# Kernel optimization log

Hardware: AMD Instinct MI355X
Metric: run time of the kernel (lower is better)

## Reference

```python
import jax, jax.numpy as jnp
import numpy as np

V, H, B, T = 128, 1024, 64, 256


def setup_inputs() -> dict:
    key = jax.random.key(0)
    ks = jax.random.split(key, 16)
    s = 0.02
    rn = lambda k, shp: (jax.random.normal(k, shp, jnp.float32) * s)
    return {
        "x": jax.random.normal(ks[0], (1, T, B, V), jnp.float32),
        "hA": jax.random.normal(ks[1], (B, H), jnp.float32),
        "cA": jax.random.normal(ks[2], (B, H), jnp.float32),
        "hB": jax.random.normal(ks[3], (B, H), jnp.float32),
        "cB": jax.random.normal(ks[4], (B, H), jnp.float32),
        "WA1": rn(ks[5], (4 * H, V)), "bA1": rn(ks[6], (4 * H,)),
        "WA2": rn(ks[7], (4 * H, H)), "bA2": rn(ks[8], (4 * H,)),
        "WB1": rn(ks[9], (4 * H, H)), "bB1": rn(ks[10], (4 * H,)),
        "WB2": rn(ks[11], (4 * H, H)), "bB2": rn(ks[12], (4 * H,)),
        "Wfc": jax.random.uniform(ks[13], (V, H), jnp.float32, -1.0, 1.0),
        "bfc": jnp.zeros((V,), jnp.float32),
    }


def _lstm_cell(x, h, c, W1, b1, W2, b2):
    # gates = Linear1(x) + Linear2(h); chunk order: in, forget, cell, out
    g = x @ W1.T + b1 + h @ W2.T + b2  # [B, 4H]
    i, f, cc, o = jnp.split(g, 4, axis=1)
    c_new = jax.nn.sigmoid(f) * c + jax.nn.sigmoid(i) * jnp.tanh(cc)
    h_new = jax.nn.sigmoid(o) * jnp.tanh(c_new)
    return h_new, c_new


def reference(x, hA, cA, hB, cB, WA1, bA1, WA2, bA2, WB1, bB1, WB2, bB2, Wfc, bfc):
    seq = x[0]  # [T, B, V], matches x.unbind(0)[0]

    def step(carry, xt):
        hA, cA, hB, cB = carry
        hA, cA = _lstm_cell(xt, hA, cA, WA1, bA1, WA2, bA2)
        hB, cB = _lstm_cell(hA, hB, cB, WB1, bB1, WB2, bB2)
        return (hA, cA, hB, cB), hB

    (hA, cA, hB, cB), outs = jax.lax.scan(step, (hA, cA, hB, cB), seq)
    # dropout is identity at inference (eval mode)
    out = outs.reshape(T * B, H) @ Wfc.T + bfc  # [T*B, V]
    return (out, hA, cA, hB, cB)
```

## Files before the change

kernel.cpp:

```cpp
#include <hip/hip_runtime.h>

#define VD 128
#define HD 1024
#define BD 64
#define TD 256
#define NB 256

typedef __bf16 bf16;
typedef __bf16 bf16x8 __attribute__((ext_vector_type(8)));
typedef __bf16 bf16x4 __attribute__((ext_vector_type(4)));
typedef float f32x4 __attribute__((ext_vector_type(4)));

#define OFF_OUTS 0ull
#define OFF_XW   33554432ull
#define OFF_WA1  (OFF_XW  + 4194304ull)
#define OFF_WA2  (OFF_WA1 + 1048576ull)
#define OFF_WB1  (OFF_WA2 + 8388608ull)
#define OFF_WB2  (OFF_WB1 + 8388608ull)
#define OFF_WFC  (OFF_WB2 + 8388608ull)
#define OFF_BUFA (OFF_WFC + 262144ull)
#define OFF_BUFB (OFF_BUFA + 262144ull)
#define OFF_CAF  (OFF_BUFB + 262144ull)
#define OFF_CBF  (OFF_CAF + 262144ull)
#define OFF_HAST (OFF_CBF + 262144ull)
#define HAST_BYTES (257ull * BD * HD * 2ull)


#define SMEM_BYTES 87040

#define BAR_WORDS 8192
#define SPIN_CAP (1 << 16)

struct Params {
  const bf16 *x, *WA1, *WA2, *WB1, *WB2;
  const float *bA1, *bA2, *bB1, *bB2;
  bf16 *bufA, *bufB, *outs;
  float *cA, *cB;
};

struct PParams {
  const bf16 *x, *WA1, *WA2, *WB1, *WB2;
  const float *bA1, *bA2, *bB1, *bB2;
  const bf16 *hBinit;
  bf16 *hAst, *outs;
  float *cA, *cB;
};

__device__ __forceinline__ bf16x8 ld8(const bf16* p) {
  return *reinterpret_cast<const bf16x8*>(p);
}
__device__ __forceinline__ float sigf(float x) { return 1.f / (1.f + __expf(-x)); }

__device__ __forceinline__ void st_dev_bf16(bf16* p, float f) {
  unsigned v = (unsigned)__builtin_bit_cast(unsigned short, (bf16)f);
  asm volatile("global_store_short %0, %1, off sc0 sc1" :: "v"(p), "v"(v) : "memory");
}

__global__ void conv_k(const float* x, const float* WA1, const float* WA2,
                       const float* WB1, const float* WB2, const float* Wfc,
                       char* ws, int sm) {
  const size_t g4 = (size_t)blockIdx.x * 256 + threadIdx.x;
  size_t i = g4 * 4;
  if (i < 2097152ull) {
    float4 v = *reinterpret_cast<const float4*>(x + i);
    bf16x4 o = { (bf16)v.x, (bf16)v.y, (bf16)v.z, (bf16)v.w };
    bf16* dst = (bf16*)(ws + OFF_XW);
    if (sm) {
      size_t t = i >> 13, r = i & 8191, b = r >> 7, vv = r & 127;
      *reinterpret_cast<bf16x4*>(dst + t * 8192 + ((vv >> 5) << 11) + (b << 5) + (vv & 31)) = o;
    } else {
      *reinterpret_cast<bf16x4*>(dst + i) = o;
    }
    return;
  }
  const float* src;
  bf16* dst;
  size_t off;
  if (i < 2621440ull)        { src = WA1; dst = (bf16*)(ws + OFF_WA1); off = i - 2097152ull; }
  else if (i < 6815744ull)   { src = WA2; dst = (bf16*)(ws + OFF_WA2); off = i - 2621440ull; }
  else if (i < 11010048ull)  { src = WB1; dst = (bf16*)(ws + OFF_WB1); off = i - 6815744ull; }
  else if (i < 15204352ull)  { src = WB2; dst = (bf16*)(ws + OFF_WB2); off = i - 11010048ull; }
  else if (i < 15335424ull)  { src = Wfc; dst = (bf16*)(ws + OFF_WFC); off = i - 15204352ull; }
  else return;
  float4 v = *reinterpret_cast<const float4*>(src + off);
  bf16x4 o = { (bf16)v.x, (bf16)v.y, (bf16)v.z, (bf16)v.w };
  *reinterpret_cast<bf16x4*>(dst + off) = o;
}

__global__ void init_k(const float* hA, const float* cA, const float* hB, const float* cB,
                       char* ws, unsigned* bar, int sm) {
  int i = blockIdx.x * 256 + threadIdx.x;
  if (i < BAR_WORDS) bar[i] = 0u;
  ((float*)(ws + OFF_CAF))[i] = cA[i];
  ((float*)(ws + OFF_CBF))[i] = cB[i];
  ((bf16*)(ws + OFF_BUFB))[i] = (bf16)hB[i];
  if (sm) {
    int b = i >> 10, j = i & 1023;
    int tix = ((j >> 5) << 11) + (b << 5) + (j & 31);
    ((bf16*)(ws + OFF_HAST))[tix] = (bf16)hA[i];
    ((bf16*)(ws + OFF_BUFA))[tix] = (bf16)hB[i];
  } else {
    ((bf16*)(ws + OFF_BUFA))[i] = (bf16)hA[i];
  }
}

__global__ void __launch_bounds__(512, 2) persist_k(PParams p, unsigned* bar) {
  extern __shared__ char smem[];
  float (*part)[8][16][65] = (float (*)[8][16][65])smem;

  const int tid = threadIdx.x;
  const int wv = tid >> 6, lane = tid & 63;
  const int lrow = lane & 15, q = lane >> 4;
  const int j0 = blockIdx.x * 4;
  const int grow = (lrow >> 2) * HD + j0 + (lrow & 3);
  const int mrow = lrow << 5;
  const int kbase = wv * 128;

  bf16x8 wa2[4], wb1[4], wb2[4], wa1 = {};
#pragma unroll
  for (int g = 0; g < 4; g++) {
    const size_t ko = (size_t)grow * HD + kbase + g * 32 + q * 8;
    wa2[g] = ld8(p.WA2 + ko);
    wb1[g] = ld8(p.WB1 + ko);
    wb2[g] = ld8(p.WB2 + ko);
  }
  if (wv < 4) wa1 = ld8(p.WA1 + (size_t)grow * VD + wv * 32 + q * 8);

  const int ejj = tid & 3;
  const int eb = (tid >> 2) & 63;
  const int ecs = tid >> 8;
  const int ej = j0 + ejj;
  const int eidx = eb * HD + ej;
  const int etix = ((ej >> 5) << 11) + (eb << 5) + (ej & 31);
  const float* b1 = ecs ? p.bB1 : p.bA1;
  const float* b2 = ecs ? p.bB2 : p.bA2;
  float* ec = ecs ? p.cB : p.cA;
  float bsum[4];
#pragma unroll
  for (int g = 0; g < 4; g++) bsum[g] = b1[g * HD + ej] + b2[g * HD + ej];
  float creg = ec[eidx];

  __syncthreads();

  for (int t = 0; t <= TD; t++) {
    const bool doA = (t < TD), doB = (t >= 1);
    const bf16* hA = p.hAst + (size_t)t * 65536;
    const bf16* hAg = hA + wv * 8192 + q * 8;
    f32x4 accA[4] = {};
    f32x4 accB[4] = {};
    bf16x8 af[4];
#pragma unroll
    for (int g = 0; g < 4; g++) {
#pragma unroll
      for (int m = 0; m < 4; m++)
        af[m] = ld8(hAg + g * 2048 + m * 512 + mrow);
      if (doA)
#pragma unroll
        for (int m = 0; m < 4; m++)
          accA[m] = __builtin_amdgcn_mfma_f32_16x16x32_bf16(af[m], wa2[g], accA[m], 0, 0, 0);
      if (doB)
#pragma unroll
        for (int m = 0; m < 4; m++)
          accB[m] = __builtin_amdgcn_mfma_f32_16x16x32_bf16(af[m], wb1[g], accB[m], 0, 0, 0);
    }
    if (doA && wv < 4) {
      const bf16* xb = p.x + (size_t)t * 8192 + wv * 2048 + q * 8;
#pragma unroll
      for (int m = 0; m < 4; m++) {
        bf16x8 xf = ld8(xb + m * 512 + mrow);
        accA[m] = __builtin_amdgcn_mfma_f32_16x16x32_bf16(xf, wa1, accA[m], 0, 0, 0);
      }
    }
    if (doB) {
      const bf16* hBb = (t == 1) ? p.hBinit : p.outs + (size_t)(t - 2) * 65536;
      const bf16* hBg = hBb + wv * 8192 + q * 8;
#pragma unroll
      for (int g = 0; g < 4; g++) {
#pragma unroll
        for (int m = 0; m < 4; m++) {
          bf16x8 bf_ = ld8(hBg + g * 2048 + m * 512 + mrow);
          accB[m] = __builtin_amdgcn_mfma_f32_16x16x32_bf16(bf_, wb2[g], accB[m], 0, 0, 0);
        }
      }
    }
    if (doA)
#pragma unroll
      for (int m = 0; m < 4; m++)
#pragma unroll
        for (int r = 0; r < 4; r++)
          part[0][wv][lrow][m * 16 + q * 4 + r] = accA[m][r];
    if (doB)
#pragma unroll
      for (int m = 0; m < 4; m++)
#pragma unroll
        for (int r = 0; r < 4; r++)
          part[1][wv][lrow][m * 16 + q * 4 + r] = accB[m][r];
    __syncthreads();

    const bool ew = (ecs == 0) ? doA : doB;
    if (ew) {
      float g4[4];
#pragma unroll
      for (int g = 0; g < 4; g++) {
        int n = g * 4 + ejj;
        float s = 0.f;
#pragma unroll
        for (int w = 0; w < 8; w++) s += part[ecs][w][n][eb];
        g4[g] = bsum[g] + s;
      }
      float cn = sigf(g4[1]) * creg + sigf(g4[0]) * tanhf(g4[2]);
      float hn = sigf(g4[3]) * tanhf(cn);
      creg = cn;
      if (ecs == 0) {
        st_dev_bf16(p.hAst + (size_t)(t + 1) * 65536 + etix, hn);
      } else {
        st_dev_bf16(p.outs + (size_t)(t - 1) * 65536 + etix, hn);
      }
    }

    if (t < TD) {
      asm volatile("s_waitcnt vmcnt(0)" ::: "memory");
      __syncthreads();
      const unsigned tgt = (unsigned)(t + 1);
      if (blockIdx.x == 0 && wv == 0) {
        if (lane == 0)
          __hip_atomic_store(&bar[1024], tgt, __ATOMIC_RELAXED, __HIP_MEMORY_SCOPE_AGENT);
        int sp = 0;
        for (;;) {
          unsigned a0 = __hip_atomic_load(&bar[1024 + (lane * 4 + 0) * 16], __ATOMIC_RELAXED, __HIP_MEMORY_SCOPE_AGENT);
          unsigned a1 = __hip_atomic_load(&bar[1024 + (lane * 4 + 1) * 16], __ATOMIC_RELAXED, __HIP_MEMORY_SCOPE_AGENT);
          unsigned a2 = __hip_atomic_load(&bar[1024 + (lane * 4 + 2) * 16], __ATOMIC_RELAXED, __HIP_MEMORY_SCOPE_AGENT);
          unsigned a3 = __hip_atomic_load(&bar[1024 + (lane * 4 + 3) * 16], __ATOMIC_RELAXED, __HIP_MEMORY_SCOPE_AGENT);
          if (__all(a0 >= tgt && a1 >= tgt && a2 >= tgt && a3 >= tgt)) break;
          __builtin_amdgcn_s_sleep(2);
          if (++sp > SPIN_CAP) break;
        }
        __hip_atomic_store(&bar[lane * 16], tgt, __ATOMIC_RELAXED, __HIP_MEMORY_SCOPE_AGENT);
      } else if (tid == 0) {
        __hip_atomic_store(&bar[1024 + blockIdx.x * 16], tgt, __ATOMIC_RELAXED, __HIP_MEMORY_SCOPE_AGENT);
        int sp = 0;
        while (__hip_atomic_load(&bar[(blockIdx.x & 63) * 16], __ATOMIC_RELAXED, __HIP_MEMORY_SCOPE_AGENT) < tgt) {
          __builtin_amdgcn_s_sleep(2);
          if (++sp > SPIN_CAP) break;
        }
      }
      __syncthreads();
    }
  }
  ec[eidx] = creg;
}

__global__ void __launch_bounds__(512) phase_k(Params p, int t) {
  __shared__ float part[8][16][65];
  const int tid = threadIdx.x;
  const int wv = tid >> 6, lane = tid & 63;
  const int lrow = lane & 15, q = lane >> 4;
  const int j0 = blockIdx.x * 4;
  const int cs = wv >> 2, kq = wv & 3;
  const int gate = lrow >> 2, jj = lrow & 3;
  const int grow = gate * HD + j0 + jj;

  const bf16 *w1, *w2;
  if (cs == 0) { w1 = p.WA1 + grow * VD + q * 8; w2 = p.WA2 + (size_t)grow * HD + q * 8; }
  else         { w1 = p.WB1 + (size_t)grow * HD + q * 8; w2 = p.WB2 + (size_t)grow * HD + q * 8; }

  const bool active = (cs == 0) ? (t < TD) : (t >= 1);
  const bf16* hA = p.bufA + ((t & 1) ? (size_t)BD * HD : 0);
  if (active) {
    f32x4 acc[4] = {};
    if (cs == 0) {
      if (kq == 0) {
        const bf16* xb = p.x + (size_t)t * BD * VD + q * 8;
#pragma unroll
        for (int s = 0; s < 4; s++) {
          bf16x8 bfv = ld8(w1 + s * 32);
          const bf16* ap = xb + s * 32;
#pragma unroll
          for (int m = 0; m < 4; m++) {
            bf16x8 afv = ld8(ap + (m * 16 + lrow) * VD);
            acc[m] = __builtin_amdgcn_mfma_f32_16x16x32_bf16(afv, bfv, acc[m], 0, 0, 0);
          }
        }
      }
      const int hk0 = (kq == 0) ? 0 : kq * 288 - 128;
      const int nh = (kq == 0) ? 5 : 9;
#pragma unroll 3
      for (int s = 0; s < nh; s++) {
        int hk = hk0 + s * 32;
        bf16x8 bfv = ld8(w2 + hk);
        const bf16* ap = hA + hk + q * 8;
#pragma unroll
        for (int m = 0; m < 4; m++) {
          bf16x8 afv = ld8(ap + (size_t)(m * 16 + lrow) * HD);
          acc[m] = __builtin_amdgcn_mfma_f32_16x16x32_bf16(afv, bfv, acc[m], 0, 0, 0);
        }
      }
    } else {
      const bf16* hB = p.bufB + (((t - 1) & 1) ? (size_t)BD * HD : 0);
      const bf16* hp = (kq < 2) ? hA : hB;
      const bf16* wp = (kq < 2) ? w1 : w2;
      const int k0 = (kq & 1) * 512;
#pragma unroll 4
      for (int s = 0; s < 16; s++) {
        int hk = k0 + s * 32;
        bf16x8 bfv = ld8(wp + hk);
        const bf16* ap = hp + hk + q * 8;
#pragma unroll
        for (int m = 0; m < 4; m++) {
          bf16x8 afv = ld8(ap + (size_t)(m * 16 + lrow) * HD);
          acc[m] = __builtin_amdgcn_mfma_f32_16x16x32_bf16(afv, bfv, acc[m], 0, 0, 0);
        }
      }
    }
#pragma unroll
    for (int m = 0; m < 4; m++)
#pragma unroll
      for (int r = 0; r < 4; r++)
        part[wv][lrow][m * 16 + q * 4 + r] = acc[m][r];
  }
  __syncthreads();

  const int eb = tid & 63;
  const int ejj = (tid >> 6) & 3;
  const int ecs = tid >> 8;
  const int ej = j0 + ejj;
  const int eidx = eb * HD + ej;
  const bool ew = (ecs == 0) ? (t < TD) : (t >= 1);
  if (ew) {
    const float* b1 = ecs ? p.bB1 : p.bA1;
    const float* b2 = ecs ? p.bB2 : p.bA2;
    float* ec = ecs ? p.cB : p.cA;
    const int wb = ecs * 4;
    float g4[4];
#pragma unroll
    for (int g = 0; g < 4; g++) {
      int n = g * 4 + ejj;
      g4[g] = b1[g * HD + ej] + b2[g * HD + ej] + part[wb + 0][n][eb] +
              part[wb + 1][n][eb] + part[wb + 2][n][eb] + part[wb + 3][n][eb];
    }
    float cold = ec[eidx];
    float cn = sigf(g4[1]) * cold + sigf(g4[0]) * tanhf(g4[2]);
    float hn = sigf(g4[3]) * tanhf(cn);
    ec[eidx] = cn;
    if (ecs == 0) {
      p.bufA[(((t + 1) & 1) ? (size_t)BD * HD : 0) + eidx] = (bf16)hn;
    } else {
      p.bufB[((t & 1) ? (size_t)BD * HD : 0) + eidx] = (bf16)hn;
      p.outs[((size_t)(t - 1) * BD + eb) * HD + ej] = (bf16)hn;
    }
  }
}

__global__ void fc_k(const bf16* outs, const bf16* Wfc, const float* bfc, float* out,
                     int sm) {
  const int tid = threadIdx.x;
  const int wv = tid >> 6, lane = tid & 63;
  const int lrow = lane & 15, q = lane >> 4;
  const int row0 = blockIdx.x * 64 + wv * 16;
  const bf16* arow;
  int astride;
  if (sm) {
    const int bb = wv * 16 + lrow;
    arow = outs + (size_t)blockIdx.x * 65536 + (bb << 5) + q * 8;
    astride = 2048;
  } else {
    arow = outs + (size_t)(row0 + lrow) * HD + q * 8;
    astride = 32;
  }
  const bf16* wrow[8];
#pragma unroll
  for (int ct = 0; ct < 8; ct++) wrow[ct] = Wfc + (size_t)(ct * 16 + lrow) * HD + q * 8;
  f32x4 acc[8] = {};
#pragma unroll 2
  for (int s = 0; s < 32; s++) {
    bf16x8 afv = ld8(arow + (size_t)s * astride);
#pragma unroll
    for (int ct = 0; ct < 8; ct++) {
      bf16x8 bfv = ld8(wrow[ct] + s * 32);
      acc[ct] = __builtin_amdgcn_mfma_f32_16x16x32_bf16(afv, bfv, acc[ct], 0, 0, 0);
    }
  }
#pragma unroll
  for (int ct = 0; ct < 8; ct++) {
    float bv = bfc[ct * 16 + lrow];
#pragma unroll
    for (int r = 0; r < 4; r++)
      out[(size_t)(row0 + q * 4 + r) * VD + ct * 16 + lrow] = acc[ct][r] + bv;
  }
}

__global__ void tail_k(const char* ws, float* out, int sm) {
  int i = blockIdx.x * 256 + threadIdx.x;
  float* o = out + (size_t)TD * BD * VD;
  float hAv, hBv;
  if (sm) {
    int b = i >> 10, j = i & 1023;
    int tix = ((j >> 5) << 11) + (b << 5) + (j & 31);
    hAv = (float)(((const bf16*)(ws + OFF_HAST))[(size_t)TD * 65536 + tix]);
    hBv = (float)(((const bf16*)(ws + OFF_OUTS))[(size_t)(TD - 1) * 65536 + tix]);
  } else {
    hAv = (float)((const bf16*)(ws + OFF_BUFA))[i];
    hBv = (float)((const bf16*)(ws + OFF_BUFB))[i];
  }
  o[i]             = hAv;
  o[65536 + i]     = ((const float*)(ws + OFF_CAF))[i];
  o[2 * 65536 + i] = hBv;
  o[3 * 65536 + i] = ((const float*)(ws + OFF_CBF))[i];
}

extern "C" void kernel_launch(void* const* d_in, const int* in_sizes, int n_in,
                              void* d_out, int out_size, void* d_ws, size_t ws_size,
                              hipStream_t stream) {
  const float* x   = (const float*)d_in[0];
  const float* hA  = (const float*)d_in[1];
  const float* cA  = (const float*)d_in[2];
  const float* hB  = (const float*)d_in[3];
  const float* cB  = (const float*)d_in[4];
  const float* WA1 = (const float*)d_in[5];
  const float* bA1 = (const float*)d_in[6];
  const float* WA2 = (const float*)d_in[7];
  const float* bA2 = (const float*)d_in[8];
  const float* WB1 = (const float*)d_in[9];
  const float* bB1 = (const float*)d_in[10];
  const float* WB2 = (const float*)d_in[11];
  const float* bB2 = (const float*)d_in[12];
  const float* Wfc = (const float*)d_in[13];
  const float* bfc = (const float*)d_in[14];

  char* ws = (char*)d_ws;
  unsigned* bar = (unsigned*)d_out;

  const int sm = (ws_size >= OFF_HAST + HAST_BYTES) ? 1 : 0;

  static bool attr_done = false;
  if (!attr_done) {
    hipFuncSetAttribute((const void*)persist_k,
                        hipFuncAttributeMaxDynamicSharedMemorySize, SMEM_BYTES);
    attr_done = true;
  }

  conv_k<<<(15335424 / 4 + 255) / 256, 256, 0, stream>>>(x, WA1, WA2, WB1, WB2, Wfc, ws, sm);
  init_k<<<256, 256, 0, stream>>>(hA, cA, hB, cB, ws, bar, sm);

  bool used_stream = false;
  if (sm) {
    PParams pp{(const bf16*)(ws + OFF_XW), (const bf16*)(ws + OFF_WA1),
               (const bf16*)(ws + OFF_WA2), (const bf16*)(ws + OFF_WB1),
               (const bf16*)(ws + OFF_WB2),
               bA1, bA2, bB1, bB2,
               (const bf16*)(ws + OFF_BUFA),
               (bf16*)(ws + OFF_HAST), (bf16*)(ws + OFF_OUTS),
               (float*)(ws + OFF_CAF), (float*)(ws + OFF_CBF)};
    persist_k<<<NB, 512, SMEM_BYTES, stream>>>(pp, bar);
    used_stream = (hipGetLastError() == hipSuccess);
  }
  if (!used_stream) {
    Params p{(const bf16*)(ws + OFF_XW), (const bf16*)(ws + OFF_WA1),
             (const bf16*)(ws + OFF_WA2), (const bf16*)(ws + OFF_WB1),
             (const bf16*)(ws + OFF_WB2),
             bA1, bA2, bB1, bB2,
             (bf16*)(ws + OFF_BUFA), (bf16*)(ws + OFF_BUFB), (bf16*)(ws + OFF_OUTS),
             (float*)(ws + OFF_CAF), (float*)(ws + OFF_CBF)};
    for (int t = 0; t <= TD; t++) {
      phase_k<<<NB, 512, 0, stream>>>(p, t);
    }
  }

  fc_k<<<256, 256, 0, stream>>>((const bf16*)(ws + OFF_OUTS), (const bf16*)(ws + OFF_WFC),
                                bfc, (float*)d_out, used_stream ? 1 : 0);
  tail_k<<<256, 256, 0, stream>>>(ws, (float*)d_out, used_stream ? 1 : 0);
}
```

Measured before the change: 2.123 ms.

## Halve persistent LSTM grid by giving each block eight hidden units

```diff
diff --git a/kernel.cpp b/kernel.cpp
--- a/kernel.cpp
+++ b/kernel.cpp
@@ -5,6 +5,7 @@
 #define BD 64
 #define TD 256
 #define NB 256
+#define NBP 128
 
 typedef __bf16 bf16;
 typedef __bf16 bf16x8 __attribute__((ext_vector_type(8)));
@@ -26,7 +27,7 @@
 #define HAST_BYTES (257ull * BD * HD * 2ull)
 
 
-#define SMEM_BYTES 87040
+#define SMEM_BYTES 134144
 
 #define BAR_WORDS 8192
 #define SPIN_CAP (1 << 16)
@@ -106,39 +107,56 @@
 
 __global__ void __launch_bounds__(512, 2) persist_k(PParams p, unsigned* bar) {
   extern __shared__ char smem[];
-  float (*part)[8][16][65] = (float (*)[8][16][65])smem;
+  float (*part)[8][16][131] = (float (*)[8][16][131])smem;
 
   const int tid = threadIdx.x;
   const int wv = tid >> 6, lane = tid & 63;
   const int lrow = lane & 15, q = lane >> 4;
-  const int j0 = blockIdx.x * 4;
-  const int grow = (lrow >> 2) * HD + j0 + (lrow & 3);
+  const int j0 = blockIdx.x * 8;
   const int mrow = lrow << 5;
   const int kbase = wv * 128;
 
-  bf16x8 wa2[4], wb1[4], wb2[4], wa1 = {};
-#pragma unroll
-  for (int g = 0; g < 4; g++) {
-    const size_t ko = (size_t)grow * HD + kbase + g * 32 + q * 8;
-    wa2[g] = ld8(p.WA2 + ko);
-    wb1[g] = ld8(p.WB1 + ko);
-    wb2[g] = ld8(p.WB2 + ko);
-  }
-  if (wv < 4) wa1 = ld8(p.WA1 + (size_t)grow * VD + wv * 32 + q * 8);
+  bf16x8 wa2[4][2], wb1[4][2], wb2[4][2];
+  bf16x8 wa1[2] = {};
+#pragma unroll
+  for (int g = 0; g < 4; g++)
+#pragma unroll
+    for (int nf = 0; nf < 2; nf++) {
+      const int grow = (lrow >> 2) * HD + j0 + nf * 4 + (lrow & 3);
+      const size_t ko = (size_t)grow * HD + kbase + g * 32 + q * 8;
+      wa2[g][nf] = ld8(p.WA2 + ko);
+      wb1[g][nf] = ld8(p.WB1 + ko);
+      wb2[g][nf] = ld8(p.WB2 + ko);
+    }
+  if (wv < 4) {
+#pragma unroll
+    for (int nf = 0; nf < 2; nf++) {
+      const int grow = (lrow >> 2) * HD + j0 + nf * 4 + (lrow & 3);
+      wa1[nf] = ld8(p.WA1 + (size_t)grow * VD + wv * 32 + q * 8);
+    }
+  }
 
   const int ejj = tid & 3;
   const int eb = (tid >> 2) & 63;
   const int ecs = tid >> 8;
-  const int ej = j0 + ejj;
-  const int eidx = eb * HD + ej;
-  const int etix = ((ej >> 5) << 11) + (eb << 5) + (ej & 31);
   const float* b1 = ecs ? p.bB1 : p.bA1;
   const float* b2 = ecs ? p.bB2 : p.bA2;
   float* ec = ecs ? p.cB : p.cA;
-  float bsum[4];
-#pragma unroll
-  for (int g = 0; g < 4; g++) bsum[g] = b1[g * HD + ej] + b2[g * HD + ej];
-  float creg = ec[eidx];
+  int eidx0, eidx1, etix0, etix1;
+  float bsum[2][4], creg[2];
+  {
+    const int ejA = j0 + ejj, ejB = j0 + 4 + ejj;
+    eidx0 = eb * HD + ejA;  eidx1 = eb * HD + ejB;
+    etix0 = ((ejA >> 5) << 11) + (eb << 5) + (ejA & 31);
+    etix1 = ((ejB >> 5) << 11) + (eb << 5) + (ejB & 31);
+#pragma unroll
+    for (int g = 0; g < 4; g++) {
+      bsum[0][g] = b1[g * HD + ejA] + b2[g * HD + ejA];
+      bsum[1][g] = b1[g * HD + ejB] + b2[g * HD + ejB];
+    }
+    creg[0] = ec[eidx0];
+    creg[1] = ec[eidx1];
+  }
 
   __syncthreads();
 
@@ -146,8 +164,8 @@
     const bool doA = (t < TD), doB = (t >= 1);
     const bf16* hA = p.hAst + (size_t)t * 65536;
     const bf16* hAg = hA + wv * 8192 + q * 8;
-    f32x4 accA[4] = {};
-    f32x4 accB[4] = {};
+    f32x4 accA[2][4] = {};
+    f32x4 accB[2][4] = {};
     bf16x8 af[4];
 #pragma unroll
     for (int g = 0; g < 4; g++) {
@@ -156,19 +174,25 @@
         af[m] = ld8(hAg + g * 2048 + m * 512 + mrow);
       if (doA)
 #pragma unroll
-        for (int m = 0; m < 4; m++)
-          accA[m] = __builtin_amdgcn_mfma_f32_16x16x32_bf16(af[m], wa2[g], accA[m], 0, 0, 0);
+        for (int nf = 0; nf < 2; nf++)
+#pragma unroll
+          for (int m = 0; m < 4; m++)
+            accA[nf][m] = __builtin_amdgcn_mfma_f32_16x16x32_bf16(af[m], wa2[g][nf], accA[nf][m], 0, 0, 0);
       if (doB)
 #pragma unroll
-        for (int m = 0; m < 4; m++)
-          accB[m] = __builtin_amdgcn_mfma_f32_16x16x32_bf16(af[m], wb1[g], accB[m], 0, 0, 0);
+        for (int nf = 0; nf < 2; nf++)
+#pragma unroll
+          for (int m = 0; m < 4; m++)
+            accB[nf][m] = __builtin_amdgcn_mfma_f32_16x16x32_bf16(af[m], wb1[g][nf], accB[nf][m], 0, 0, 0);
     }
     if (doA && wv < 4) {
       const bf16* xb = p.x + (size_t)t * 8192 + wv * 2048 + q * 8;
 #pragma unroll
       for (int m = 0; m < 4; m++) {
         bf16x8 xf = ld8(xb + m * 512 + mrow);
-        accA[m] = __builtin_amdgcn_mfma_f32_16x16x32_bf16(xf, wa1, accA[m], 0, 0, 0);
+#pragma unroll
+        for (int nf = 0; nf < 2; nf++)
+          accA[nf][m] = __builtin_amdgcn_mfma_f32_16x16x32_bf16(xf, wa1[nf], accA[nf][m], 0, 0, 0);
       }
     }
     if (doB) {
@@ -179,42 +203,53 @@
 #pragma unroll
         for (int m = 0; m < 4; m++) {
           bf16x8 bf_ = ld8(hBg + g * 2048 + m * 512 + mrow);
-          accB[m] = __builtin_amdgcn_mfma_f32_16x16x32_bf16(bf_, wb2[g], accB[m], 0, 0, 0);
+#pragma unroll
+          for (int nf = 0; nf < 2; nf++)
+            accB[nf][m] = __builtin_amdgcn_mfma_f32_16x16x32_bf16(bf_, wb2[g][nf], accB[nf][m], 0, 0, 0);
         }
       }
     }
     if (doA)
 #pragma unroll
-      for (int m = 0; m < 4; m++)
-#pragma unroll
-        for (int r = 0; r < 4; r++)
-          part[0][wv][lrow][m * 16 + q * 4 + r] = accA[m][r];
+      for (int nf = 0; nf < 2; nf++)
+#pragma unroll
+        for (int m = 0; m < 4; m++)
+#pragma unroll
+          for (int r = 0; r < 4; r++)
+            part[0][wv][lrow][nf * 65 + m * 16 + q * 4 + r] = accA[nf][m][r];
     if (doB)
 #pragma unroll
-      for (int m = 0; m < 4; m++)
-#pragma unroll
-        for (int r = 0; r < 4; r++)
-          part[1][wv][lrow][m * 16 + q * 4 + r] = accB[m][r];
+      for (int nf = 0; nf < 2; nf++)
+#pragma unroll
+        for (int m = 0; m < 4; m++)
+#pragma unroll
+          for (int r = 0; r < 4; r++)
+            part[1][wv][lrow][nf * 65 + m * 16 + q * 4 + r] = accB[nf][m][r];
     __syncthreads();
 
     const bool ew = (ecs == 0) ? doA : doB;
     if (ew) {
-      float g4[4];
-#pragma unroll
-      for (int g = 0; g < 4; g++) {
-        int n = g * 4 + ejj;
-        float s = 0.f;
-#pragma unroll
-        for (int w = 0; w < 8; w++) s += part[ecs][w][n][eb];
-        g4[g] = bsum[g] + s;
-      }
-      float cn = sigf(g4[1]) * creg + sigf(g4[0]) * tanhf(g4[2]);
-      float hn = sigf(g4[3]) * tanhf(cn);
-      creg = cn;
-      if (ecs == 0) {
-        st_dev_bf16(p.hAst + (size_t)(t + 1) * 65536 + etix, hn);
-      } else {
-        st_dev_bf16(p.outs + (size_t)(t - 1) * 65536 + etix, hn);
+#pragma unroll
+      for (int nf = 0; nf < 2; nf++) {
+        float g4[4];
+#pragma unroll
+        for (int g = 0; g < 4; g++) {
+          int n = g * 4 + ejj;
+          float s = 0.f;
+#pragma unroll
+          for (int w = 0; w < 8; w++) s += part[ecs][w][n][nf * 65 + eb];
+          g4[g] = bsum[nf][g] + s;
+        }
+        float cr = nf ? creg[1] : creg[0];
+        float cn = sigf(g4[1]) * cr + sigf(g4[0]) * tanhf(g4[2]);
+        float hn = sigf(g4[3]) * tanhf(cn);
+        if (nf) creg[1] = cn; else creg[0] = cn;
+        const int et = nf ? etix1 : etix0;
+        if (ecs == 0) {
+          st_dev_bf16(p.hAst + (size_t)(t + 1) * 65536 + et, hn);
+        } else {
+          st_dev_bf16(p.outs + (size_t)(t - 1) * 65536 + et, hn);
+        }
       }
     }
 
@@ -227,11 +262,9 @@
           __hip_atomic_store(&bar[1024], tgt, __ATOMIC_RELAXED, __HIP_MEMORY_SCOPE_AGENT);
         int sp = 0;
         for (;;) {
-          unsigned a0 = __hip_atomic_load(&bar[1024 + (lane * 4 + 0) * 16], __ATOMIC_RELAXED, __HIP_MEMORY_SCOPE_AGENT);
-          unsigned a1 = __hip_atomic_load(&bar[1024 + (lane * 4 + 1) * 16], __ATOMIC_RELAXED, __HIP_MEMORY_SCOPE_AGENT);
-          unsigned a2 = __hip_atomic_load(&bar[1024 + (lane * 4 + 2) * 16], __ATOMIC_RELAXED, __HIP_MEMORY_SCOPE_AGENT);
-          unsigned a3 = __hip_atomic_load(&bar[1024 + (lane * 4 + 3) * 16], __ATOMIC_RELAXED, __HIP_MEMORY_SCOPE_AGENT);
-          if (__all(a0 >= tgt && a1 >= tgt && a2 >= tgt && a3 >= tgt)) break;
+          unsigned a0 = __hip_atomic_load(&bar[1024 + (lane * 2 + 0) * 16], __ATOMIC_RELAXED, __HIP_MEMORY_SCOPE_AGENT);
+          unsigned a1 = __hip_atomic_load(&bar[1024 + (lane * 2 + 1) * 16], __ATOMIC_RELAXED, __HIP_MEMORY_SCOPE_AGENT);
+          if (__all(a0 >= tgt && a1 >= tgt)) break;
           __builtin_amdgcn_s_sleep(2);
           if (++sp > SPIN_CAP) break;
         }
@@ -247,7 +280,8 @@
       __syncthreads();
     }
   }
-  ec[eidx] = creg;
+  ec[eidx0] = creg[0];
+  ec[eidx1] = creg[1];
 }
 
 __global__ void __launch_bounds__(512) phase_k(Params p, int t) {
@@ -451,7 +485,7 @@
                (const bf16*)(ws + OFF_BUFA),
                (bf16*)(ws + OFF_HAST), (bf16*)(ws + OFF_OUTS),
                (float*)(ws + OFF_CAF), (float*)(ws + OFF_CBF)};
-    persist_k<<<NB, 512, SMEM_BYTES, stream>>>(pp, bar);
+    persist_k<<<NBP, 512, SMEM_BYTES, stream>>>(pp, bar);
     used_stream = (hipGetLastError() == hipSuccess);
   }
   if (!used_stream) {
```

Result: slower. 2.423 ms (+14.1%).
